# Optimization experiments

Measured on AMD Instinct MI355X. Metric: run time of the kernel, lower is better.

## Reference

```python
import jax, jax.numpy as jnp
import numpy as np

B, S, HID, H = 8, 128, 256, 4
DH = HID // H
FF = 4 * HID


def setup_inputs() -> dict:
    key = jax.random.key(0)
    ks = jax.random.split(key, 16)
    n = lambda i, shape: jax.random.normal(ks[i], shape, dtype=jnp.float32) * 0.02
    z = lambda shape: jnp.zeros(shape, dtype=jnp.float32)
    return dict(
        x=jax.random.normal(ks[0], (B, S, HID), dtype=jnp.float32),
        attention_mask=jnp.zeros((B, 1, S, S), dtype=jnp.float32),
        Wq=n(1, (HID, HID)), bq=z((HID,)),
        Wk=n(2, (HID, HID)), bk=z((HID,)),
        Wv=n(3, (HID, HID)), bv=z((HID,)),
        order_w=n(4, (2 * DH,)), order_b=z(()),
        dist_w=n(5, (2 * DH,)), dist_b=z(()),
        scalar=jax.random.normal(ks[6], (1,), dtype=jnp.float32),
        AWq=n(7, (HID, HID)), Abq=z((HID,)),
        AWk=n(8, (HID, HID)), Abk=z((HID,)),
        Wd=n(9, (HID, HID)), bd=z((HID,)),
        g1=jnp.ones((HID,), jnp.float32), beta1=z((HID,)),
        W1=n(10, (HID, FF)), b1=z((FF,)),
        W2=n(11, (FF, HID)), b2=z((HID,)),
        g2=jnp.ones((HID,), jnp.float32), beta2=z((HID,)),
    )


def _ln(t, g, b, eps=1e-12):
    m = t.mean(-1, keepdims=True)
    v = ((t - m) ** 2).mean(-1, keepdims=True)
    return (t - m) / jnp.sqrt(v + eps) * g + b


def _heads(t):
    # [B,S,HID] -> [B,H,S,DH]
    return t.reshape(B, S, H, DH).transpose(0, 2, 1, 3)


def reference(x, attention_mask, Wq, bq, Wk, bk, Wv, bv, order_w, order_b,
              dist_w, dist_b, scalar, AWq, Abq, AWk, Abk, Wd, bd,
              g1, beta1, W1, b1, W2, b2, g2, beta2):
    inv = 1.0 / jnp.sqrt(jnp.float32(DH))
    q = x @ Wq + bq
    k = x @ Wk + bk
    v = x @ Wv + bv
    qh, kh, vh = _heads(q), _heads(k), _heads(v)
    scores = jnp.einsum('bhqd,bhkd->bhqk', qh, kh)  # [B,H,S,S]

    # order/distance affines on concat(q_i, k_j): Linear(2*DH,1) decomposes into
    # per-token projections summed via broadcast (same math, no [B,H,S,S,2*DH] tensor)
    pr_order = jax.nn.sigmoid((qh @ order_w[:DH])[..., :, None]
                              + (kh @ order_w[DH:])[..., None, :] + order_b)
    gd_order = jnp.triu(jnp.ones((S, S), jnp.float32), k=1)
    err_order = (jnp.log(pr_order + 1e-24) * gd_order
                 + jnp.log(1.0 - pr_order + 1e-24) * (1.0 - gd_order))

    idx = jnp.arange(S)
    gd_dist = jnp.log(jnp.abs(idx[None, :] - idx[:, None]).astype(jnp.float32) + 1.0)
    pr_dist = ((qh @ dist_w[:DH])[..., :, None]
               + (kh @ dist_w[DH:])[..., None, :] + dist_b)
    err_dist = -jnp.square(gd_dist - pr_dist) * jnp.square(scalar[0]) * 0.5

    rich_scores = scores + err_order + err_dist
    softm = lambda s: jax.nn.softmax(s * inv + attention_mask, axis=-1)
    rich_probs = softm(rich_scores)
    origin_probs = softm(scores)

    # rich/calibrated combine ('fixed'): softmax(origin + 0.5 * rich)
    combined = jax.nn.softmax(origin_probs + 0.5 * rich_probs, axis=-1)

    # two-level attack attention on transformed mixed q/k
    aq, ak = _heads(q @ AWq + Abq), _heads(k @ AWk + Abk)
    attack_probs = softm(jnp.einsum('bhqd,bhkd->bhqk', aq, ak))
    final_probs = jax.nn.softmax(combined + 0.5 * attack_probs, axis=-1)

    ctx = jnp.einsum('bhqk,bhkd->bhqd', final_probs, vh)
    ctx = ctx.transpose(0, 2, 1, 3).reshape(B, S, HID)
    h = _ln(ctx @ Wd + bd + x, g1, beta1)
    f = jax.nn.gelu(h @ W1 + b1, approximate=False) @ W2 + b2
    return _ln(f + h, g2, beta2)
```

## Files before the change

kernel.cpp:

```cpp
#include <hip/hip_runtime.h>
#include <hip/hip_bf16.h>
#include <math.h>

#define B_  8
#define S_  128
#define HID_ 256
#define H_  4
#define DH_ 64
#define FF_ 1024
#define M_  (B_ * S_)

typedef _Float16 half_t;
typedef __attribute__((ext_vector_type(8))) _Float16 half8;
typedef __attribute__((ext_vector_type(4))) float floatx4;

enum { EP_F32 = 0, EP_F16 = 1, EP_F16B = 2, EP_GELU = 3, EP_PROJ = 4 };

__device__ __forceinline__ floatx4 mfma16(half8 a, half8 b, floatx4 c) {
    return __builtin_amdgcn_mfma_f32_16x16x32_f16(a, b, c, 0, 0, 0);
}

__device__ __forceinline__ float wred_sum(float v) {
#pragma unroll
    for (int o = 32; o >= 1; o >>= 1) v += __shfl_xor(v, o, 64);
    return v;
}
__device__ __forceinline__ float block_sum_256(float v, float* s4, int tid) {
    v = wred_sum(v);
    __syncthreads();
    if ((tid & 63) == 0) s4[tid >> 6] = v;
    __syncthreads();
    return s4[0] + s4[1] + s4[2] + s4[3];
}
__device__ __forceinline__ float qred_sum(float v) {
#pragma unroll
    for (int o = 1; o < 16; o <<= 1) v += __shfl_xor(v, o, 64);
    return v;
}
__device__ __forceinline__ void sm8(float (&v)[8]) {
    float s = 0.f;
#pragma unroll
    for (int j = 0; j < 8; ++j) { v[j] = __expf(v[j]); s += v[j]; }
    s = qred_sum(s);
    float r = 1.f / s;
#pragma unroll
    for (int j = 0; j < 8; ++j) v[j] *= r;
}

template<int EPI>
__device__ __forceinline__ void mgemm(
    const half_t* __restrict__ A, int ldA,
    const half_t* __restrict__ Bt, int ldB,
    int kLen, int m0, int n0,
    const float* __restrict__ bias,
    float* __restrict__ Cf, half_t* __restrict__ Ch, int ldC,
    const float* __restrict__ pw1, const float* __restrict__ pw2,
    float* __restrict__ po1, float* __restrict__ po2, int hsel)
{
    __shared__ half8 Asf[2][4][64];
    __shared__ half8 Bsf[2][4][64];

    const int tid = threadIdx.x;
    const int w = tid >> 6, l = tid & 63;
    const int sr = tid >> 2;
    const int sq = tid & 3;
    const int sdst = (sr & 15) | (sq << 4);
    const int smt = sr >> 4;
    const half_t* Ap = A + (size_t)(m0 + sr) * ldA + sq * 8;
    const half_t* Bp = Bt + (size_t)(n0 + sr) * ldB + sq * 8;

    half8 ra, rb;
    auto fetch = [&](int t) {
        ra = *(const half8*)(Ap + t * 32);
        rb = *(const half8*)(Bp + t * 32);
    };
    auto commit = [&](int buf) {
        Asf[buf][smt][sdst] = ra;
        Bsf[buf][smt][sdst] = rb;
    };

    floatx4 zero = {0.f, 0.f, 0.f, 0.f};
    floatx4 acc[4] = {zero, zero, zero, zero};
    const int kt = kLen >> 5;

    fetch(0);
    commit(0);
    __syncthreads();
    for (int t = 0; t < kt; ++t) {
        const bool more = (t + 1 < kt);
        if (more) fetch(t + 1);
        const int buf = t & 1;
        half8 a = Asf[buf][w][l];
        acc[0] = mfma16(a, Bsf[buf][0][l], acc[0]);
        acc[1] = mfma16(a, Bsf[buf][1][l], acc[1]);
        acc[2] = mfma16(a, Bsf[buf][2][l], acc[2]);
        acc[3] = mfma16(a, Bsf[buf][3][l], acc[3]);
        if (more) {
            commit((t + 1) & 1);
            __syncthreads();
        }
    }

    const int quad = l >> 4, lc = l & 15;
    const int rowb = m0 + w * 16 + quad * 4;
    float bvv[4] = {0.f, 0.f, 0.f, 0.f};
    if (EPI >= EP_F16B) {
#pragma unroll
        for (int nt = 0; nt < 4; ++nt) bvv[nt] = bias[n0 + nt * 16 + lc];
    }
    float pw1v[4], pw2v[4];
    if (EPI == EP_PROJ) {
#pragma unroll
        for (int nt = 0; nt < 4; ++nt) {
            pw1v[nt] = pw1[nt * 16 + lc];
            pw2v[nt] = pw2[nt * 16 + lc];
        }
    }
#pragma unroll
    for (int rr = 0; rr < 4; ++rr) {
        float ov[4];
#pragma unroll
        for (int nt = 0; nt < 4; ++nt) {
            float o = acc[nt][rr];
            if (EPI >= EP_F16B) o += bvv[nt];
            if (EPI == EP_GELU) o = 0.5f * o * (1.f + erff(o * 0.70710678118654752f));
            ov[nt] = o;
            const size_t ci = (size_t)(rowb + rr) * ldC + n0 + nt * 16 + lc;
            if (EPI == EP_F32) Cf[ci] = o;
            else Ch[ci] = (half_t)o;
        }
        if (EPI == EP_PROJ) {
            float po = ov[0] * pw1v[0] + ov[1] * pw1v[1] + ov[2] * pw1v[2] + ov[3] * pw1v[3];
            float pd = ov[0] * pw2v[0] + ov[1] * pw2v[1] + ov[2] * pw2v[2] + ov[3] * pw2v[3];
#pragma unroll
            for (int off = 1; off < 16; off <<= 1) {
                po += __shfl_xor(po, off, 64);
                pd += __shfl_xor(pd, off, 64);
            }
            if (lc == 0) {
                const int m = rowb + rr;
                const int idx = ((m >> 7) * H_ + hsel) * S_ + (m & 127);
                po1[idx] = po;
                po2[idx] = pd;
            }
        }
    }
}

__global__ __launch_bounds__(256) void prep_kernel(
    const float* __restrict__ x,
    const float* __restrict__ Wq, const float* __restrict__ Wk,
    const float* __restrict__ Wv, const float* __restrict__ Wd,
    const float* __restrict__ AWq, const float* __restrict__ AWk,
    const float* __restrict__ W1, const float* __restrict__ W2,
    half_t* __restrict__ x16, half_t* __restrict__ Wq16n, half_t* __restrict__ Wk16n,
    half_t* __restrict__ WqT, half_t* __restrict__ WkT, half_t* __restrict__ WvT,
    half_t* __restrict__ WdT, half_t* __restrict__ AWqT, half_t* __restrict__ AWkT,
    half_t* __restrict__ W1T, half_t* __restrict__ W2T)
{
    const int z = blockIdx.z, bx = blockIdx.x, by = blockIdx.y;
    const int tid = threadIdx.x;
    if (z < 3) {
        const float* src = (z == 0) ? x : (z == 1) ? Wq : Wk;
        half_t* dst = (z == 0) ? x16 : (z == 1) ? Wq16n : Wk16n;
        const int total = (z == 0) ? M_ * HID_ : HID_ * HID_;
        const int bid = by * 16 + bx;
        if (bid * 1024 < total) {
            const int base = bid * 1024 + tid * 4;
            float4 vv = *(const float4*)(src + base);
            dst[base + 0] = (half_t)vv.x;
            dst[base + 1] = (half_t)vv.y;
            dst[base + 2] = (half_t)vv.z;
            dst[base + 3] = (half_t)vv.w;
        }
        return;
    }
    const float* src; half_t* dst; int K, N, k0, n0;
    if (z <= 8) {
        const float* ins[6] = {Wq, Wk, Wv, Wd, AWq, AWk};
        half_t* outs[6] = {WqT, WkT, WvT, WdT, AWqT, AWkT};
        src = ins[z - 3]; dst = outs[z - 3];
        K = 256; N = 256; k0 = bx * 64; n0 = by * 64;
        if (bx >= 4 || by >= 4) return;
    } else if (z == 9) {
        src = W1; dst = W1T; K = 256; N = 1024;
        k0 = bx * 64; n0 = by * 64;
        if (bx >= 4) return;
    } else {
        src = W2; dst = W2T; K = 1024; N = 256;
        k0 = by * 64; n0 = bx * 64;
        if (bx >= 4) return;
    }
    __shared__ half_t tl[64][72];
    const int r = tid >> 2, c0 = (tid & 3) * 16;
#pragma unroll 4
    for (int i = 0; i < 16; ++i)
        tl[c0 + i][r] = (half_t)src[(size_t)(k0 + r) * N + n0 + c0 + i];
    __syncthreads();
#pragma unroll 4
    for (int i = 0; i < 16; ++i)
        dst[(size_t)(n0 + r) * K + k0 + c0 + i] = tl[r][c0 + i];
}

__global__ __launch_bounds__(256) void compose_mfma(
    const half_t* __restrict__ AWqT, const half_t* __restrict__ AWkT,
    const half_t* __restrict__ Wq16n, const half_t* __restrict__ Wk16n,
    const float* __restrict__ AWq, const float* __restrict__ AWk,
    const float* __restrict__ bq, const float* __restrict__ bk,
    const float* __restrict__ Abq, const float* __restrict__ Abk,
    half_t* __restrict__ WcqT, half_t* __restrict__ WckT,
    float* __restrict__ bcq, float* __restrict__ bck)
{
    const int z = blockIdx.z;
    if (blockIdx.y < 4) {
        const half_t* A = z ? AWkT : AWqT;
        const half_t* Bt = z ? Wk16n : Wq16n;
        half_t* C = z ? WckT : WcqT;
        mgemm<EP_F16>(A, HID_, Bt, HID_, HID_, blockIdx.y * 64, blockIdx.x * 64,
                      nullptr, nullptr, C, HID_, nullptr, nullptr, nullptr, nullptr, 0);
    } else {
        __shared__ float red[4][64];
        const float* bsrc = z ? bk : bq;
        const float* AW   = z ? AWk : AWq;
        const float* Ab   = z ? Abk : Abq;
        float* bco        = z ? bck : bcq;
        int t = threadIdx.x, l = t & 63, kc = t >> 6;
        int n = blockIdx.x * 64 + l;
        float p = 0.f;
#pragma unroll 8
        for (int kk = 0; kk < 64; ++kk) {
            int k = kc * 64 + kk;
            p = fmaf(bsrc[k], AW[(size_t)k * HID_ + n], p);
        }
        red[kc][l] = p;
        __syncthreads();
        if (kc == 0)
            bco[n] = red[0][l] + red[1][l] + red[2][l] + red[3][l] + Ab[n];
    }
}

__global__ __launch_bounds__(256) void xgemm5(
    const half_t* __restrict__ x16,
    const half_t* __restrict__ WqT, const float* __restrict__ bq,
    const half_t* __restrict__ WkT, const float* __restrict__ bk,
    const half_t* __restrict__ WvT, const float* __restrict__ bv,
    const half_t* __restrict__ WcqT, const float* __restrict__ bcq,
    const half_t* __restrict__ WckT, const float* __restrict__ bck,
    const float* __restrict__ order_w, const float* __restrict__ dist_w,
    half_t* __restrict__ q16, half_t* __restrict__ k16, half_t* __restrict__ v16,
    half_t* __restrict__ aq16, half_t* __restrict__ ak16,
    float* __restrict__ qoA, float* __restrict__ qdA,
    float* __restrict__ koA, float* __restrict__ kdA)
{
    const int z = blockIdx.z;
    const int m0 = blockIdx.y * 64, n0 = blockIdx.x * 64;
    if (z == 0)
        mgemm<EP_PROJ>(x16, HID_, WqT, HID_, HID_, m0, n0, bq, nullptr, q16, HID_,
                       order_w, dist_w, qoA, qdA, blockIdx.x);
    else if (z == 1)
        mgemm<EP_PROJ>(x16, HID_, WkT, HID_, HID_, m0, n0, bk, nullptr, k16, HID_,
                       order_w + DH_, dist_w + DH_, koA, kdA, blockIdx.x);
    else if (z == 2)
        mgemm<EP_F16B>(x16, HID_, WvT, HID_, HID_, m0, n0, bv, nullptr, v16, HID_,
                       nullptr, nullptr, nullptr, nullptr, 0);
    else if (z == 3)
        mgemm<EP_F16B>(x16, HID_, WcqT, HID_, HID_, m0, n0, bcq, nullptr, aq16, HID_,
                       nullptr, nullptr, nullptr, nullptr, 0);
    else
        mgemm<EP_F16B>(x16, HID_, WckT, HID_, HID_, m0, n0, bck, nullptr, ak16, HID_,
                       nullptr, nullptr, nullptr, nullptr, 0);
}

__global__ __launch_bounds__(64) void attn_fused(
    const half_t* __restrict__ q16, const half_t* __restrict__ k16,
    const half_t* __restrict__ v16, const half_t* __restrict__ aq16,
    const half_t* __restrict__ ak16,
    const float* __restrict__ qoA, const float* __restrict__ qdA,
    const float* __restrict__ koA, const float* __restrict__ kdA,
    const float* __restrict__ mask,
    const float* __restrict__ order_b_p, const float* __restrict__ dist_b_p,
    const float* __restrict__ scalar_p,
    half_t* __restrict__ ctx16)
{
    __shared__ half8 Qf[2][64], AQf[2][64];
    __shared__ half8 Kf[2][8][64], AKf[2][8][64];
    __shared__ half_t Vt[64][136];
    __shared__ half_t Pm[16][136];

    const int l = threadIdx.x;
    const int quad = l >> 4, lc = l & 15;
    const int bh = blockIdx.x >> 3, rt = blockIdx.x & 7;
    const int b = bh >> 2, h = bh & 3;
    const size_t hoff = (size_t)b * S_ * HID_ + h * DH_;

#pragma unroll
    for (int u = 0; u < 2; ++u) {
        int idx = u * 64 + l;
        int r = idx >> 3, c = idx & 7;
        size_t g = hoff + (size_t)(rt * 16 + r) * HID_ + c * 8;
        int kt = c >> 2, sl = r | ((c & 3) << 4);
        Qf[kt][sl]  = *(const half8*)(q16 + g);
        AQf[kt][sl] = *(const half8*)(aq16 + g);
    }
#pragma unroll
    for (int u = 0; u < 16; ++u) {
        int idx = u * 64 + l;
        int j = idx >> 3, c = idx & 7;
        size_t g = hoff + (size_t)j * HID_ + c * 8;
        int kt = c >> 2, jt = j >> 4, sl = (j & 15) | ((c & 3) << 4);
        Kf[kt][jt][sl]  = *(const half8*)(k16 + g);
        AKf[kt][jt][sl] = *(const half8*)(ak16 + g);
    }
#pragma unroll
    for (int u = 0; u < 16; ++u) {
        int j = (u >> 3) * 64 + l;
        int c = u & 7;
        half8 vv = *(const half8*)(v16 + hoff + (size_t)j * HID_ + c * 8);
#pragma unroll
        for (int e = 0; e < 8; ++e) Vt[c * 8 + e][j] = vv[e];
    }
    __syncthreads();

    floatx4 zero = {0.f, 0.f, 0.f, 0.f};
    floatx4 accS[8], accA[8];
#pragma unroll
    for (int jt = 0; jt < 8; ++jt) { accS[jt] = zero; accA[jt] = zero; }
#pragma unroll
    for (int kt = 0; kt < 2; ++kt) {
        half8 a0 = Qf[kt][l];
        half8 a1 = AQf[kt][l];
#pragma unroll
        for (int jt = 0; jt < 8; ++jt) {
            accS[jt] = mfma16(a0, Kf[kt][jt][l], accS[jt]);
            accA[jt] = mfma16(a1, AKf[kt][jt][l], accA[jt]);
        }
    }

    const float ob = order_b_p[0], db = dist_b_p[0];
    const float scl = scalar_p[0];
    const float s2 = scl * scl;
    const float inv = 0.125f;
    float kov[8], kdv[8];
#pragma unroll
    for (int jt = 0; jt < 8; ++jt) {
        kov[jt] = koA[bh * S_ + jt * 16 + lc];
        kdv[jt] = kdA[bh * S_ + jt * 16 + lc];
    }
#pragma unroll
    for (int reg = 0; reg < 4; ++reg) {
        const int il = quad * 4 + reg;
        const int i  = rt * 16 + il;
        float qo = qoA[bh * S_ + i], qd = qdA[bh * S_ + i];
        const float* mrow = mask + ((size_t)(b * S_ + i)) * S_;
        float mk[8], lg[8], as_[8];
#pragma unroll
        for (int jt = 0; jt < 8; ++jt) {
            mk[jt] = mrow[jt * 16 + lc];
            lg[jt] = accS[jt][reg];
            as_[jt] = accA[jt][reg];
        }
        float p0[8];
#pragma unroll
        for (int jt = 0; jt < 8; ++jt) p0[jt] = lg[jt] * inv + mk[jt];
        sm8(p0);
        float p1[8];
#pragma unroll
        for (int jt = 0; jt < 8; ++jt) {
            int j = jt * 16 + lc;
            float pr = 1.f / (1.f + __expf(-(qo + kov[jt] + ob)));
            float sel = (j > i) ? pr : 1.f - pr;
            float erro = __logf(sel + 1e-24f);
            float gd = __logf(fabsf((float)(j - i)) + 1.f);
            float dd = gd - (qd + kdv[jt] + db);
            p1[jt] = (lg[jt] + erro - 0.5f * dd * dd * s2) * inv + mk[jt];
        }
        sm8(p1);
#pragma unroll
        for (int jt = 0; jt < 8; ++jt) p0[jt] += 0.5f * p1[jt];
        sm8(p0);
#pragma unroll
        for (int jt = 0; jt < 8; ++jt) p1[jt] = as_[jt] * inv + mk[jt];
        sm8(p1);
#pragma unroll
        for (int jt = 0; jt < 8; ++jt) p0[jt] += 0.5f * p1[jt];
        sm8(p0);
#pragma unroll
        for (int jt = 0; jt < 8; ++jt) Pm[il][jt * 16 + lc] = (half_t)p0[jt];
    }
    __syncthreads();

    half8 pa_[4];
#pragma unroll
    for (int kt = 0; kt < 4; ++kt)
        pa_[kt] = *(const half8*)&Pm[lc][kt * 32 + quad * 8];
    floatx4 apv[4];
#pragma unroll
    for (int nt = 0; nt < 4; ++nt) apv[nt] = zero;
#pragma unroll
    for (int nt = 0; nt < 4; ++nt) {
#pragma unroll
        for (int kt = 0; kt < 4; ++kt) {
            half8 vf = *(const half8*)&Vt[nt * 16 + lc][kt * 32 + quad * 8];
            apv[nt] = mfma16(pa_[kt], vf, apv[nt]);
        }
    }
#pragma unroll
    for (int nt = 0; nt < 4; ++nt) {
#pragma unroll
        for (int reg = 0; reg < 4; ++reg) {
            int i = rt * 16 + quad * 4 + reg;
            ctx16[hoff + (size_t)i * HID_ + nt * 16 + lc] = (half_t)apv[nt][reg];
        }
    }
}

__global__ __launch_bounds__(256) void dense_mfma(
    const half_t* __restrict__ ctx16, const half_t* __restrict__ WdT,
    float* __restrict__ dn)
{
    mgemm<EP_F32>(ctx16, HID_, WdT, HID_, HID_, blockIdx.y * 64, blockIdx.x * 64,
                  nullptr, dn, nullptr, HID_, nullptr, nullptr, nullptr, nullptr, 0);
}

__global__ __launch_bounds__(256) void ff1_mfma(
    const half_t* __restrict__ h16, const half_t* __restrict__ W1T,
    const float* __restrict__ b1, half_t* __restrict__ f116)
{
    mgemm<EP_GELU>(h16, HID_, W1T, HID_, HID_, blockIdx.y * 64, blockIdx.x * 64,
                   b1, nullptr, f116, FF_, nullptr, nullptr, nullptr, nullptr, 0);
}

__global__ __launch_bounds__(256) void ff2_mfma(
    const half_t* __restrict__ f116, const half_t* __restrict__ W2T,
    float* __restrict__ p0, float* __restrict__ p1,
    float* __restrict__ p2, float* __restrict__ p3)
{
    const int z = blockIdx.z;
    float* C = (z == 0) ? p0 : (z == 1) ? p1 : (z == 2) ? p2 : p3;
    mgemm<EP_F32>(f116 + z * 256, FF_, W2T + z * 256, FF_, 256,
                  blockIdx.y * 64, blockIdx.x * 64,
                  nullptr, C, nullptr, HID_, nullptr, nullptr, nullptr, nullptr, 0);
}

__global__ __launch_bounds__(256) void ln1_kernel(
    const float* __restrict__ dn, const float* __restrict__ bd,
    const float* __restrict__ x,
    const float* __restrict__ g1, const float* __restrict__ beta1,
    float* __restrict__ h32, half_t* __restrict__ h16)
{
    __shared__ float s4[4];
    const int row = blockIdx.x;
    const int n = threadIdx.x;
    const size_t idx = (size_t)row * HID_ + n;
    float val = dn[idx] + bd[n] + x[idx];
    float mean = block_sum_256(val, s4, n) * (1.f / HID_);
    float dv = val - mean;
    float var = block_sum_256(dv * dv, s4, n) * (1.f / HID_);
    float r = dv * rsqrtf(var + 1e-12f) * g1[n] + beta1[n];
    h32[idx] = r;
    h16[idx] = (half_t)r;
}

__global__ __launch_bounds__(256) void ln2_kernel(
    const float* __restrict__ p0, const float* __restrict__ p1,
    const float* __restrict__ p2, const float* __restrict__ p3,
    const float* __restrict__ b2, const float* __restrict__ h32,
    const float* __restrict__ g2, const float* __restrict__ beta2,
    float* __restrict__ out)
{
    __shared__ float s4[4];
    const int row = blockIdx.x;
    const int n = threadIdx.x;
    const size_t idx = (size_t)row * HID_ + n;
    float val = p0[idx] + p1[idx] + p2[idx] + p3[idx] + b2[n] + h32[idx];
    float mean = block_sum_256(val, s4, n) * (1.f / HID_);
    float dv = val - mean;
    float var = block_sum_256(dv * dv, s4, n) * (1.f / HID_);
    out[idx] = dv * rsqrtf(var + 1e-12f) * g2[n] + beta2[n];
}

extern "C" void kernel_launch(void* const* d_in, const int* in_sizes, int n_in,
                              void* d_out, int out_size, void* d_ws, size_t ws_size,
                              hipStream_t stream) {
    const float* x        = (const float*)d_in[0];
    const float* mask     = (const float*)d_in[1];
    const float* Wq       = (const float*)d_in[2];
    const float* bq       = (const float*)d_in[3];
    const float* Wk       = (const float*)d_in[4];
    const float* bk       = (const float*)d_in[5];
    const float* Wv       = (const float*)d_in[6];
    const float* bv       = (const float*)d_in[7];
    const float* order_w  = (const float*)d_in[8];
    const float* order_b  = (const float*)d_in[9];
    const float* dist_w   = (const float*)d_in[10];
    const float* dist_b   = (const float*)d_in[11];
    const float* scalar   = (const float*)d_in[12];
    const float* AWq      = (const float*)d_in[13];
    const float* Abq      = (const float*)d_in[14];
    const float* AWk      = (const float*)d_in[15];
    const float* Abk      = (const float*)d_in[16];
    const float* Wd       = (const float*)d_in[17];
    const float* bd       = (const float*)d_in[18];
    const float* g1       = (const float*)d_in[19];
    const float* beta1    = (const float*)d_in[20];
    const float* W1       = (const float*)d_in[21];
    const float* b1       = (const float*)d_in[22];
    const float* W2       = (const float*)d_in[23];
    const float* b2       = (const float*)d_in[24];
    const float* g2       = (const float*)d_in[25];
    const float* beta2    = (const float*)d_in[26];

    float* ws = (float*)d_ws;
    size_t off = 0;
    auto afl = [&](size_t n) { float* p = ws + off; off += n; return p; };
    auto ahf = [&](size_t nh) { half_t* p = (half_t*)(ws + off); off += nh / 2; return p; };

    half_t* x16   = ahf(M_ * HID_);
    half_t* Wq16n = ahf(HID_ * HID_);
    half_t* Wk16n = ahf(HID_ * HID_);
    half_t* WqT   = ahf(HID_ * HID_);
    half_t* WkT   = ahf(HID_ * HID_);
    half_t* WvT   = ahf(HID_ * HID_);
    half_t* WdT   = ahf(HID_ * HID_);
    half_t* AWqT  = ahf(HID_ * HID_);
    half_t* AWkT  = ahf(HID_ * HID_);
    half_t* W1T   = ahf(HID_ * FF_);
    half_t* W2T   = ahf(HID_ * FF_);
    half_t* WcqT  = ahf(HID_ * HID_);
    half_t* WckT  = ahf(HID_ * HID_);
    half_t* q16   = ahf(M_ * HID_);
    half_t* k16   = ahf(M_ * HID_);
    half_t* v16   = ahf(M_ * HID_);
    half_t* aq16  = ahf(M_ * HID_);
    half_t* ak16  = ahf(M_ * HID_);
    half_t* ctx16 = ahf(M_ * HID_);
    half_t* h16   = ahf(M_ * HID_);
    half_t* f116  = ahf(M_ * FF_);
    float* dnb  = afl(M_ * HID_);
    float* hb32 = afl(M_ * HID_);
    float* pf0  = afl(M_ * HID_);
    float* pf1  = afl(M_ * HID_);
    float* pf2  = afl(M_ * HID_);
    float* pf3  = afl(M_ * HID_);
    float* bcq  = afl(256);
    float* bck  = afl(256);
    float* qoA  = afl(B_ * H_ * S_);
    float* qdA  = afl(B_ * H_ * S_);
    float* koA  = afl(B_ * H_ * S_);
    float* kdA  = afl(B_ * H_ * S_);

    prep_kernel<<<dim3(16, 16, 11), 256, 0, stream>>>(
        x, Wq, Wk, Wv, Wd, AWq, AWk, W1, W2,
        x16, Wq16n, Wk16n, WqT, WkT, WvT, WdT, AWqT, AWkT, W1T, W2T);
    compose_mfma<<<dim3(4, 5, 2), 256, 0, stream>>>(
        AWqT, AWkT, Wq16n, Wk16n, AWq, AWk, bq, bk, Abq, Abk, WcqT, WckT, bcq, bck);
    xgemm5<<<dim3(4, 16, 5), 256, 0, stream>>>(
        x16, WqT, bq, WkT, bk, WvT, bv, WcqT, bcq, WckT, bck, order_w, dist_w,
        q16, k16, v16, aq16, ak16, qoA, qdA, koA, kdA);
    attn_fused<<<256, 64, 0, stream>>>(
        q16, k16, v16, aq16, ak16, qoA, qdA, koA, kdA,
        mask, order_b, dist_b, scalar, ctx16);
    dense_mfma<<<dim3(4, 16), 256, 0, stream>>>(ctx16, WdT, dnb);
    ln1_kernel<<<M_, 256, 0, stream>>>(dnb, bd, x, g1, beta1, hb32, h16);
    ff1_mfma<<<dim3(16, 16), 256, 0, stream>>>(h16, W1T, b1, f116);
    ff2_mfma<<<dim3(4, 16, 4), 256, 0, stream>>>(f116, W2T, pf0, pf1, pf2, pf3);
    ln2_kernel<<<M_, 256, 0, stream>>>(pf0, pf1, pf2, pf3, b2, hb32, g2, beta2, (float*)d_out);
}
```

Before: 162.4 us.

## Write V transposed from projection GEMM and use wave-per-row LayerNorms

The V projection epilogue now writes V directly in a per-head transposed [b,h,d,s] layout. This lets the attention kernel load Vt rows with contiguous half8 copies instead of scattering 8 scalar LDS stores per load. Both LayerNorm kernels now process one row per wavefront with float4 loads and shuffle-only reductions, so they drop the shared-memory block reductions and barriers and launch 4x fewer blocks. The transposed epilogue issues narrower strided half4 global stores in the GEMM.

```diff
diff --git a/kernel.cpp b/kernel.cpp
--- a/kernel.cpp
+++ b/kernel.cpp
@@ -11,10 +11,11 @@
 #define M_  (B_ * S_)
 
 typedef _Float16 half_t;
+typedef __attribute__((ext_vector_type(4))) _Float16 half4;
 typedef __attribute__((ext_vector_type(8))) _Float16 half8;
 typedef __attribute__((ext_vector_type(4))) float floatx4;
 
-enum { EP_F32 = 0, EP_F16 = 1, EP_F16B = 2, EP_GELU = 3, EP_PROJ = 4 };
+enum { EP_F32 = 0, EP_F16 = 1, EP_F16B = 2, EP_GELU = 3, EP_PROJ = 4, EP_VT = 5 };
 
 __device__ __forceinline__ floatx4 mfma16(half8 a, half8 b, floatx4 c) {
     return __builtin_amdgcn_mfma_f32_16x16x32_f16(a, b, c, 0, 0, 0);
@@ -24,13 +25,6 @@
 #pragma unroll
     for (int o = 32; o >= 1; o >>= 1) v += __shfl_xor(v, o, 64);
     return v;
-}
-__device__ __forceinline__ float block_sum_256(float v, float* s4, int tid) {
-    v = wred_sum(v);
-    __syncthreads();
-    if ((tid & 63) == 0) s4[tid >> 6] = v;
-    __syncthreads();
-    return s4[0] + s4[1] + s4[2] + s4[3];
 }
 __device__ __forceinline__ float qred_sum(float v) {
 #pragma unroll
@@ -107,6 +101,20 @@
     if (EPI >= EP_F16B) {
 #pragma unroll
         for (int nt = 0; nt < 4; ++nt) bvv[nt] = bias[n0 + nt * 16 + lc];
+    }
+    if (EPI == EP_VT) {
+        const int b = rowb >> 7;
+        const int jb = rowb & 127;
+        const int h = n0 >> 6;
+#pragma unroll
+        for (int nt = 0; nt < 4; ++nt) {
+            const int d = nt * 16 + lc;
+            half4 v4;
+#pragma unroll
+            for (int rr = 0; rr < 4; ++rr) v4[rr] = (half_t)(acc[nt][rr] + bvv[nt]);
+            *(half4*)(Ch + (((size_t)b * H_ + h) * 64 + d) * 128 + jb) = v4;
+        }
+        return;
     }
     float pw1v[4], pw2v[4];
     if (EPI == EP_PROJ) {
@@ -247,7 +255,7 @@
     const half_t* __restrict__ WcqT, const float* __restrict__ bcq,
     const half_t* __restrict__ WckT, const float* __restrict__ bck,
     const float* __restrict__ order_w, const float* __restrict__ dist_w,
-    half_t* __restrict__ q16, half_t* __restrict__ k16, half_t* __restrict__ v16,
+    half_t* __restrict__ q16, half_t* __restrict__ k16, half_t* __restrict__ vt16,
     half_t* __restrict__ aq16, half_t* __restrict__ ak16,
     float* __restrict__ qoA, float* __restrict__ qdA,
     float* __restrict__ koA, float* __restrict__ kdA)
@@ -261,8 +269,8 @@
         mgemm<EP_PROJ>(x16, HID_, WkT, HID_, HID_, m0, n0, bk, nullptr, k16, HID_,
                        order_w + DH_, dist_w + DH_, koA, kdA, blockIdx.x);
     else if (z == 2)
-        mgemm<EP_F16B>(x16, HID_, WvT, HID_, HID_, m0, n0, bv, nullptr, v16, HID_,
-                       nullptr, nullptr, nullptr, nullptr, 0);
+        mgemm<EP_VT>(x16, HID_, WvT, HID_, HID_, m0, n0, bv, nullptr, vt16, HID_,
+                     nullptr, nullptr, nullptr, nullptr, 0);
     else if (z == 3)
         mgemm<EP_F16B>(x16, HID_, WcqT, HID_, HID_, m0, n0, bcq, nullptr, aq16, HID_,
                        nullptr, nullptr, nullptr, nullptr, 0);
@@ -273,7 +281,7 @@
 
 __global__ __launch_bounds__(64) void attn_fused(
     const half_t* __restrict__ q16, const half_t* __restrict__ k16,
-    const half_t* __restrict__ v16, const half_t* __restrict__ aq16,
+    const half_t* __restrict__ vt16, const half_t* __restrict__ aq16,
     const half_t* __restrict__ ak16,
     const float* __restrict__ qoA, const float* __restrict__ qdA,
     const float* __restrict__ koA, const float* __restrict__ kdA,
@@ -313,11 +321,10 @@
     }
 #pragma unroll
     for (int u = 0; u < 16; ++u) {
-        int j = (u >> 3) * 64 + l;
-        int c = u & 7;
-        half8 vv = *(const half8*)(v16 + hoff + (size_t)j * HID_ + c * 8);
-#pragma unroll
-        for (int e = 0; e < 8; ++e) Vt[c * 8 + e][j] = vv[e];
+        int idx = u * 64 + l;
+        int d = idx >> 4, jc = idx & 15;
+        half8 vv = *(const half8*)(vt16 + ((size_t)bh * 64 + d) * 128 + jc * 8);
+        *(half8*)&Vt[d][jc * 8] = vv;
     }
     __syncthreads();
 
@@ -448,17 +455,33 @@
     const float* __restrict__ g1, const float* __restrict__ beta1,
     float* __restrict__ h32, half_t* __restrict__ h16)
 {
-    __shared__ float s4[4];
-    const int row = blockIdx.x;
-    const int n = threadIdx.x;
-    const size_t idx = (size_t)row * HID_ + n;
-    float val = dn[idx] + bd[n] + x[idx];
-    float mean = block_sum_256(val, s4, n) * (1.f / HID_);
-    float dv = val - mean;
-    float var = block_sum_256(dv * dv, s4, n) * (1.f / HID_);
-    float r = dv * rsqrtf(var + 1e-12f) * g1[n] + beta1[n];
-    h32[idx] = r;
-    h16[idx] = (half_t)r;
+    const int w = threadIdx.x >> 6, l = threadIdx.x & 63;
+    const int row = blockIdx.x * 4 + w;
+    const size_t ro = (size_t)row * HID_ + l * 4;
+    float4 dv4 = *(const float4*)(dn + ro);
+    float4 bd4 = *(const float4*)(bd + l * 4);
+    float4 x4  = *(const float4*)(x + ro);
+    float v0 = dv4.x + bd4.x + x4.x;
+    float v1 = dv4.y + bd4.y + x4.y;
+    float v2 = dv4.z + bd4.z + x4.z;
+    float v3 = dv4.w + bd4.w + x4.w;
+    float s = wred_sum(v0 + v1 + v2 + v3);
+    float mean = s * (1.f / HID_);
+    v0 -= mean; v1 -= mean; v2 -= mean; v3 -= mean;
+    float sq = wred_sum(v0 * v0 + v1 * v1 + v2 * v2 + v3 * v3);
+    float rstd = rsqrtf(sq * (1.f / HID_) + 1e-12f);
+    float4 g4 = *(const float4*)(g1 + l * 4);
+    float4 be4 = *(const float4*)(beta1 + l * 4);
+    float4 o;
+    o.x = v0 * rstd * g4.x + be4.x;
+    o.y = v1 * rstd * g4.y + be4.y;
+    o.z = v2 * rstd * g4.z + be4.z;
+    o.w = v3 * rstd * g4.w + be4.w;
+    *(float4*)(h32 + ro) = o;
+    half4 h4v;
+    h4v[0] = (half_t)o.x; h4v[1] = (half_t)o.y;
+    h4v[2] = (half_t)o.z; h4v[3] = (half_t)o.w;
+    *(half4*)(h16 + ro) = h4v;
 }
 
 __global__ __launch_bounds__(256) void ln2_kernel(
@@ -468,15 +491,32 @@
     const float* __restrict__ g2, const float* __restrict__ beta2,
     float* __restrict__ out)
 {
-    __shared__ float s4[4];
-    const int row = blockIdx.x;
-    const int n = threadIdx.x;
-    const size_t idx = (size_t)row * HID_ + n;
-    float val = p0[idx] + p1[idx] + p2[idx] + p3[idx] + b2[n] + h32[idx];
-    float mean = block_sum_256(val, s4, n) * (1.f / HID_);
-    float dv = val - mean;
-    float var = block_sum_256(dv * dv, s4, n) * (1.f / HID_);
-    out[idx] = dv * rsqrtf(var + 1e-12f) * g2[n] + beta2[n];
+    const int w = threadIdx.x >> 6, l = threadIdx.x & 63;
+    const int row = blockIdx.x * 4 + w;
+    const size_t ro = (size_t)row * HID_ + l * 4;
+    float4 p04 = *(const float4*)(p0 + ro);
+    float4 p14 = *(const float4*)(p1 + ro);
+    float4 p24 = *(const float4*)(p2 + ro);
+    float4 p34 = *(const float4*)(p3 + ro);
+    float4 b24 = *(const float4*)(b2 + l * 4);
+    float4 h4  = *(const float4*)(h32 + ro);
+    float v0 = p04.x + p14.x + p24.x + p34.x + b24.x + h4.x;
+    float v1 = p04.y + p14.y + p24.y + p34.y + b24.y + h4.y;
+    float v2 = p04.z + p14.z + p24.z + p34.z + b24.z + h4.z;
+    float v3 = p04.w + p14.w + p24.w + p34.w + b24.w + h4.w;
+    float s = wred_sum(v0 + v1 + v2 + v3);
+    float mean = s * (1.f / HID_);
+    v0 -= mean; v1 -= mean; v2 -= mean; v3 -= mean;
+    float sq = wred_sum(v0 * v0 + v1 * v1 + v2 * v2 + v3 * v3);
+    float rstd = rsqrtf(sq * (1.f / HID_) + 1e-12f);
+    float4 g4 = *(const float4*)(g2 + l * 4);
+    float4 be4 = *(const float4*)(beta2 + l * 4);
+    float4 o;
+    o.x = v0 * rstd * g4.x + be4.x;
+    o.y = v1 * rstd * g4.y + be4.y;
+    o.z = v2 * rstd * g4.z + be4.z;
+    o.w = v3 * rstd * g4.w + be4.w;
+    *(float4*)(out + ro) = o;
 }
 
 extern "C" void kernel_launch(void* const* d_in, const int* in_sizes, int n_in,
@@ -530,7 +570,7 @@
     half_t* WckT  = ahf(HID_ * HID_);
     half_t* q16   = ahf(M_ * HID_);
     half_t* k16   = ahf(M_ * HID_);
-    half_t* v16   = ahf(M_ * HID_);
+    half_t* vt16  = ahf(M_ * HID_);
     half_t* aq16  = ahf(M_ * HID_);
     half_t* ak16  = ahf(M_ * HID_);
     half_t* ctx16 = ahf(M_ * HID_);
@@ -556,13 +596,13 @@
         AWqT, AWkT, Wq16n, Wk16n, AWq, AWk, bq, bk, Abq, Abk, WcqT, WckT, bcq, bck);
     xgemm5<<<dim3(4, 16, 5), 256, 0, stream>>>(
         x16, WqT, bq, WkT, bk, WvT, bv, WcqT, bcq, WckT, bck, order_w, dist_w,
-        q16, k16, v16, aq16, ak16, qoA, qdA, koA, kdA);
+        q16, k16, vt16, aq16, ak16, qoA, qdA, koA, kdA);
     attn_fused<<<256, 64, 0, stream>>>(
-        q16, k16, v16, aq16, ak16, qoA, qdA, koA, kdA,
+        q16, k16, vt16, aq16, ak16, qoA, qdA, koA, kdA,
         mask, order_b, dist_b, scalar, ctx16);
     dense_mfma<<<dim3(4, 16), 256, 0, stream>>>(ctx16, WdT, dnb);
-    ln1_kernel<<<M_, 256, 0, stream>>>(dnb, bd, x, g1, beta1, hb32, h16);
+    ln1_kernel<<<256, 256, 0, stream>>>(dnb, bd, x, g1, beta1, hb32, h16);
     ff1_mfma<<<dim3(16, 16), 256, 0, stream>>>(h16, W1T, b1, f116);
     ff2_mfma<<<dim3(4, 16, 4), 256, 0, stream>>>(f116, W2T, pf0, pf1, pf2, pf3);
-    ln2_kernel<<<M_, 256, 0, stream>>>(pf0, pf1, pf2, pf3, b2, hb32, g2, beta2, (float*)d_out);
-}
+    ln2_kernel<<<256, 256, 0, stream>>>(pf0, pf1, pf2, pf3, b2, hb32, g2, beta2, (float*)d_out);
+}
```

Result: no change. 162.8 us (+0.3%).
